# Optimization experiments

Measured on AMD Instinct MI355X. Metric: run time of the kernel, lower is better.

## Reference

```python
import jax, jax.numpy as jnp
import numpy as np
import math

B, NB, NA, NC, D, E, H = 4, 2048, 1024, 1024, 1024, 8, 16
HD = D // H
TOP_K = 2
T_MAX = 1000.0
TAU_MIN, TAU_MAX = 0.5, 2.0
W_MIN, W_MAX = 0.1, 0.2
CAP_LO, CAP_HI = 0.5, 0.6
FLOOR = min(0.05, 0.15 / E)       # cfg.routing_floor property
ALPHA = min(FLOOR * E, 1.0)       # routing-floor interpolation weight
BIAS_COEFF = 0.01
EPS = 1e-8


def _layernorm(x, g, b, eps=1e-5):
    mu = x.mean(-1, keepdims=True)
    var = ((x - mu) ** 2).mean(-1, keepdims=True)
    return (x - mu) * jax.lax.rsqrt(var + eps) * g + b


def _forward(tokens_B, output_A, output_C, in_proj_w, in_proj_b, out_proj_w, out_proj_b,
             ln_g, ln_b, te_w1, te_b1, te_w2, te_b2,
             gate_w1, gate_b1, gate_w2, gate_b2, expert_bias, t):
    t_norm = t.astype(jnp.float32) / T_MAX                 # (B,)
    ctx_C = jax.lax.stop_gradient(output_C)                # stopgrad_C_to_B
    ctx_AC = jnp.concatenate([output_A, ctx_C], axis=1)    # (B, NA+NC, D)

    # --- cross attention (torch nn.MultiheadAttention, batch_first) ---
    wq, wk, wv = jnp.split(in_proj_w, 3, axis=0)
    bq, bk, bv = jnp.split(in_proj_b, 3)
    q = (tokens_B @ wq.T + bq).reshape(B, NB, H, HD)
    k = (ctx_AC @ wk.T + bk).reshape(B, NA + NC, H, HD)
    v = (ctx_AC @ wv.T + bv).reshape(B, NA + NC, H, HD)
    scores = jnp.einsum('bqhd,bkhd->bhqk', q, k) / math.sqrt(HD)
    attn = jax.nn.softmax(scores, axis=-1)
    ctx = jnp.einsum('bhqk,bkhd->bqhd', attn, v).reshape(B, NB, D)
    ctx_B = ctx @ out_proj_w.T + out_proj_b
    ctx_B = _layernorm(ctx_B + tokens_B, ln_g, ln_b)

    # --- sinusoidal timestep embedding + 2-layer MLP ---
    half = D // 2
    freq = jnp.exp(-math.log(10000.0) * jnp.arange(half, dtype=jnp.float32) / (half - 1))
    args = t.astype(jnp.float32)[:, None] * freq
    emb = jnp.concatenate([jnp.sin(args), jnp.cos(args)], axis=-1)   # (B, D)
    t_emb = jax.nn.silu(emb @ te_w1.T + te_b1) @ te_w2.T + te_b2     # (B, D)
    t_emb = jnp.broadcast_to(t_emb[:, None, :], (B, NB, D))

    # --- gate MLP + expert bias + temperature ---
    gate_in = jnp.concatenate([tokens_B, ctx_B, t_emb], axis=-1)     # (B, NB, 3D)
    logits = jax.nn.relu(gate_in @ gate_w1.T + gate_b1) @ gate_w2.T + gate_b2 + expert_bias
    tau = (TAU_MIN + (TAU_MAX - TAU_MIN) * t_norm)[:, None, None]
    probs = jax.nn.softmax(logits / tau, axis=-1)                    # (B, NB, E)

    # routing floor: interpolate toward uniform
    probs = (1.0 - ALPHA) * probs + ALPHA / E

    # shared expert injection: expert 0 gets scheduled weight w(t), rest renormalised
    w = (W_MIN + (W_MAX - W_MIN) * t_norm)[:, None, None]
    shared = jnp.maximum(probs[..., 0:1], w)
    others = probs[..., 1:]
    others = others / jnp.maximum(others.sum(-1, keepdims=True), EPS) * (1.0 - shared)
    probs = jnp.concatenate([shared, others], axis=-1)

    # top-k mask (keep top-k probs, zero the rest)
    vals, idx = jax.lax.top_k(probs, TOP_K)
    dispatch = (jax.nn.one_hot(idx, E, dtype=probs.dtype) * vals[..., None]).sum(-2)

    # token-level hard cap (torch.no_grad -> stop_gradient) with redistribution
    cap = (CAP_LO + (CAP_HI - CAP_LO) * t_norm)[:, None, None]
    excess = jax.nn.relu(dispatch - cap)
    capped = dispatch - excess
    headroom = jax.nn.relu(cap - capped)
    head_sum = jnp.maximum(headroom.sum(-1, keepdims=True), EPS)
    capped = capped + excess.sum(-1, keepdims=True) * (headroom / head_sum)
    dispatch = jax.lax.stop_gradient(capped)

    # batch-level utilisation penalty on specialists 1..E-1
    fair = NB / max(E - 1, 1)
    load = dispatch.sum(axis=1).mean(axis=0)                          # (E,)
    pen_excess = jax.nn.relu(load[1:] - fair * 1.5)
    bias_penalty = BIAS_COEFF * jnp.sum(pen_excess ** 2)

    combine = dispatch / (dispatch.sum(-1, keepdims=True) + EPS)
    return dispatch, combine, bias_penalty


def setup_inputs() -> dict:
    key = jax.random.key(0)
    ks = jax.random.split(key, 12)
    g = lambda k, sh: jax.random.normal(k, sh, jnp.float32) * 0.02
    return dict(
        tokens_B=jax.random.normal(ks[0], (B, NB, D), jnp.float32),
        output_A=jax.random.normal(ks[1], (B, NA, D), jnp.float32),
        output_C=jax.random.normal(ks[2], (B, NC, D), jnp.float32),
        t=jax.random.randint(ks[3], (B,), 0, 1000, jnp.int32),
        in_proj_w=g(ks[4], (3 * D, D)),
        in_proj_b=jnp.zeros((3 * D,), jnp.float32),
        out_proj_w=g(ks[5], (D, D)),
        out_proj_b=jnp.zeros((D,), jnp.float32),
        ln_g=jnp.ones((D,), jnp.float32),
        ln_b=jnp.zeros((D,), jnp.float32),
        te_w1=g(ks[6], (2 * D, D)),
        te_b1=jnp.zeros((2 * D,), jnp.float32),
        te_w2=g(ks[7], (D, 2 * D)),
        te_b2=jnp.zeros((D,), jnp.float32),
        gate_w1=g(ks[8], (D, 3 * D)),
        gate_b1=jnp.zeros((D,), jnp.float32),
        gate_w2=g(ks[9], (E, D)),
        gate_b2=jnp.zeros((E,), jnp.float32),
        expert_bias=jnp.zeros((E,), jnp.float32),
    )


def reference(tokens_B, output_A, output_C, t, in_proj_w, in_proj_b, out_proj_w, out_proj_b,
              ln_g, ln_b, te_w1, te_b1, te_w2, te_b2,
              gate_w1, gate_b1, gate_w2, gate_b2, expert_bias):
    return _forward(tokens_B, output_A, output_C, in_proj_w, in_proj_b, out_proj_w, out_proj_b,
                    ln_g, ln_b, te_w1, te_b1, te_w2, te_b2,
                    gate_w1, gate_b1, gate_w2, gate_b2, expert_bias, t)
```

## Files before the change

### kernel.cpp

```cpp
#include <hip/hip_runtime.h>
#include <math.h>


typedef __attribute__((ext_vector_type(8))) short short8;
typedef __attribute__((ext_vector_type(4))) float f32x4;
typedef __attribute__((ext_vector_type(4))) unsigned int u32x4;
typedef unsigned short u16;
typedef unsigned int u32;

__global__ void zero_k(double* p) {
    if (threadIdx.x < 8) p[threadIdx.x] = 0.0;
}

__device__ inline u16 bf_hi(float x) {
    u32 u = __float_as_uint(x);
    u += 0x7FFFu + ((u >> 16) & 1u);
    return (u16)(u >> 16);
}
__device__ inline u16 bf_lo(float x, u16 h) {
    float hf = __uint_as_float(((u32)h) << 16);
    return bf_hi(x - hf);
}
__device__ inline u32 pack_bf(float x) {
    u32 u = __float_as_uint(x);
    u32 hi = (u + (0x7FFFu + ((u >> 16) & 1u))) >> 16;
    float hf = __uint_as_float(hi << 16);
    float d = x - hf;
    u32 u2 = __float_as_uint(d);
    u32 lo = (u2 + (0x7FFFu + ((u2 >> 16) & 1u))) >> 16;
    return (hi << 16) | lo;
}

__device__ inline void pack2(float p0, float p1, u32& o0, u32& o1) {
    u32 h01, l01;
    asm("v_cvt_pk_bf16_f32 %0, %1, %2" : "=v"(h01) : "v"(p0), "v"(p1));
    float d0 = p0 - __uint_as_float(h01 << 16);
    float d1 = p1 - __uint_as_float(h01 & 0xffff0000u);
    asm("v_cvt_pk_bf16_f32 %0, %1, %2" : "=v"(l01) : "v"(d0), "v"(d1));
    o0 = __builtin_amdgcn_perm(h01, l01, 0x05040100u);
    o1 = __builtin_amdgcn_perm(h01, l01, 0x07060302u);
}

__device__ inline void async16(const u16* g, u16* l) {
    __builtin_amdgcn_global_load_lds(
        (const __attribute__((address_space(1))) unsigned int*)g,
        (__attribute__((address_space(3))) unsigned int*)l,
        16, 0, 0);
}

__global__ __launch_bounds__(256)
void split_k(const float* __restrict__ in, u16* __restrict__ hi,
             u16* __restrict__ lo, int n4) {
    int i = blockIdx.x * 256 + threadIdx.x;
    if (i >= n4) return;
    float4 x = ((const float4*)in)[i];
    ushort4 h, l;
    h.x = bf_hi(x.x); l.x = bf_lo(x.x, h.x);
    h.y = bf_hi(x.y); l.y = bf_lo(x.y, h.y);
    h.z = bf_hi(x.z); l.z = bf_lo(x.z, h.z);
    h.w = bf_hi(x.w); l.w = bf_lo(x.w, h.w);
    ((ushort4*)hi)[i] = h;
    ((ushort4*)lo)[i] = l;
}

__global__ void emb_k(const int* __restrict__ t, float* __restrict__ emb) {
    int b = blockIdx.x;
    int j = threadIdx.x;
    float x1 = (float)(-9.210340371976184) * (float)j;
    float x2 = x1 / 511.0f;
    float freq = (float)exp((double)x2);
    float tf = (float)t[b];
    float arg = tf * freq;
    emb[b * 1024 + j]       = (float)sin((double)arg);
    emb[b * 1024 + 512 + j] = (float)cos((double)arg);
}

__global__ void te_fc_k(const float* __restrict__ in, const float* __restrict__ W,
                        const float* __restrict__ bias, float* __restrict__ out,
                        int K, int N, int do_silu) {
    int b = blockIdx.x;
    int wv = threadIdx.x >> 6, lane = threadIdx.x & 63;
    const float* inb = in + (size_t)b * K;
    int n0 = blockIdx.y * 16 + wv * 4;
    for (int q = 0; q < 4; q++) {
        int n = n0 + q;
        const float* wr = W + (size_t)n * K;
        float acc = 0.f;
        for (int c = lane * 4; c < K; c += 256) {
            float4 a  = *(const float4*)(inb + c);
            float4 w4 = *(const float4*)(wr + c);
            acc += a.x * w4.x + a.y * w4.y + a.z * w4.z + a.w * w4.w;
        }
#pragma unroll
        for (int off = 1; off < 64; off <<= 1) acc += __shfl_xor(acc, off, 64);
        if (lane == 0) {
            float x = acc + bias[n];
            out[(size_t)b * N + n] = do_silu ? (x / (1.0f + expf(-x))) : x;
        }
    }
}

template<bool GATE, bool RELU, int OMODE>
__global__ __launch_bounds__(256, 2)
void bfgemm_k(const u16* __restrict__ A0h, const u16* __restrict__ A0l,
              const u16* __restrict__ A1h, const u16* __restrict__ A1l,
              const u16* __restrict__ A2h, const u16* __restrict__ A2l,
              const u16* __restrict__ Wh_g, const u16* __restrict__ Wl_g,
              const float* __restrict__ bias, float* __restrict__ C,
              u16* __restrict__ Chi, u16* __restrict__ Clo, int K, float scale)
{
    __shared__ u16 Ah[128 * 32];
    __shared__ u16 Al[128 * 32];
    __shared__ u16 Wh[128 * 32];
    __shared__ u16 Wl[128 * 32];
    const int tid = threadIdx.x;
    const int row0 = blockIdx.x * 128;
    const int col0 = blockIdx.y * 128;
    const int wv = tid >> 6;
    const int lane = tid & 63;
    const int wrow = (wv & 1) * 64;
    const int wcol = (wv >> 1) * 64;
    const int l15 = lane & 15, quad = lane >> 4;

    f32x4 acc[4][4];
#pragma unroll
    for (int i = 0; i < 4; i++)
#pragma unroll
        for (int j = 0; j < 4; j++)
            acc[i][j] = (f32x4){0.f, 0.f, 0.f, 0.f};

    const int ar0 = tid >> 2, ak0 = (tid & 3) * 8;
    const int ar1 = (tid + 256) >> 2, ak1 = ((tid + 256) & 3) * 8;

    for (int kc = 0; kc < K; kc += 32) {
        const u16* pAh = A0h;
        const u16* pAl = A0l;
        int kk = kc;
        int tembseg = 0;
        if (GATE) {
            int seg = kc >> 10;
            if (seg == 1) { pAh = A1h; pAl = A1l; }
            else if (seg == 2) { pAh = A2h; pAl = A2l; tembseg = 1; }
            kk = kc & 1023;
        }
        const int astr = GATE ? 1024 : K;
        int g0 = row0 + ar0, g1 = row0 + ar1;
        if (GATE && tembseg) { g0 >>= 11; g1 >>= 11; }
        uint4 vah0 = *(const uint4*)&pAh[(size_t)g0 * astr + kk + ak0];
        uint4 vah1 = *(const uint4*)&pAh[(size_t)g1 * astr + kk + ak1];
        uint4 val0 = *(const uint4*)&pAl[(size_t)g0 * astr + kk + ak0];
        uint4 val1 = *(const uint4*)&pAl[(size_t)g1 * astr + kk + ak1];
        uint4 vwh0 = *(const uint4*)&Wh_g[(size_t)(col0 + ar0) * K + kc + ak0];
        uint4 vwh1 = *(const uint4*)&Wh_g[(size_t)(col0 + ar1) * K + kc + ak1];
        uint4 vwl0 = *(const uint4*)&Wl_g[(size_t)(col0 + ar0) * K + kc + ak0];
        uint4 vwl1 = *(const uint4*)&Wl_g[(size_t)(col0 + ar1) * K + kc + ak1];
        __syncthreads();
        *(uint4*)&Ah[ar0 * 32 + ak0] = vah0;
        *(uint4*)&Ah[ar1 * 32 + ak1] = vah1;
        *(uint4*)&Al[ar0 * 32 + ak0] = val0;
        *(uint4*)&Al[ar1 * 32 + ak1] = val1;
        *(uint4*)&Wh[ar0 * 32 + ak0] = vwh0;
        *(uint4*)&Wh[ar1 * 32 + ak1] = vwh1;
        *(uint4*)&Wl[ar0 * 32 + ak0] = vwl0;
        *(uint4*)&Wl[ar1 * 32 + ak1] = vwl1;
        __syncthreads();

        short8 a_h[4], a_l[4];
#pragma unroll
        for (int i = 0; i < 4; i++) {
            int r = (wrow + i * 16 + l15) * 32 + quad * 8;
            a_h[i] = *(const short8*)&Ah[r];
            a_l[i] = *(const short8*)&Al[r];
        }
#pragma unroll
        for (int j = 0; j < 4; j++) {
            int c = (wcol + j * 16 + l15) * 32 + quad * 8;
            short8 b_h = *(const short8*)&Wh[c];
            short8 b_l = *(const short8*)&Wl[c];
#pragma unroll
            for (int i = 0; i < 4; i++) {
                acc[i][j] = __builtin_amdgcn_mfma_f32_16x16x32_bf16(a_h[i], b_h, acc[i][j], 0, 0, 0);
                acc[i][j] = __builtin_amdgcn_mfma_f32_16x16x32_bf16(a_h[i], b_l, acc[i][j], 0, 0, 0);
                acc[i][j] = __builtin_amdgcn_mfma_f32_16x16x32_bf16(a_l[i], b_h, acc[i][j], 0, 0, 0);
            }
        }
    }

#pragma unroll
    for (int i = 0; i < 4; i++) {
#pragma unroll
        for (int j = 0; j < 4; j++) {
            int cc = col0 + wcol + j * 16 + l15;
#pragma unroll
            for (int r = 0; r < 4; r++) {
                int rr = row0 + wrow + i * 16 + quad * 4 + r;
                float v = (acc[i][j][r] + ((OMODE == 3) ? bias[rr] : bias[cc])) * scale;
                if (RELU) v = fmaxf(v, 0.f);
                if (OMODE == 0) {
                    C[(size_t)rr * 1024 + cc] = v;
                } else if (OMODE == 1) {
                    u32 pk = pack_bf(v);
                    size_t a = (size_t)rr * 1024 + cc;
                    Chi[a] = (u16)(pk >> 16); Clo[a] = (u16)pk;
                } else if (OMODE == 2) {
                    int orow = ((rr >> 10) & 3) * 2048 + (rr >> 12) * 1024 + (rr & 1023);
                    u32 pk = pack_bf(v);
                    size_t a = (size_t)orow * 1024 + cc;
                    Chi[a] = (u16)(pk >> 16); Clo[a] = (u16)pk;
                } else {
                    int bb2 = (cc >> 10) & 3;
                    int key = (cc >> 12) * 1024 + (cc & 1023);
                    u32 pk = pack_bf(v);
                    size_t a = ((size_t)(bb2 * 1024 + rr)) * 2048 + key;
                    Chi[a] = (u16)(pk >> 16); Clo[a] = (u16)pk;
                }
            }
        }
    }
}

__global__ __launch_bounds__(256)
void attn_k(const u16* Qh, const u16* Ql,
            const u16* __restrict__ Kh, const u16* __restrict__ Kl,
            const u16* __restrict__ Vh, const u16* __restrict__ Vl,
            u16* Oh, u16* Ol)
{
    __shared__ u32 Pu[128 * 64];
    __shared__ u16 Vsm[2][64 * 64];
    u16* Ksh = (u16*)Pu;
    u16* Ksl = Ksh + 64 * 64;

    const int tid = threadIdx.x;
    const int w = tid >> 6, lane = tid & 63;
    const int l15 = lane & 15, quad = lane >> 4;
    const int bh = blockIdx.x, b = bh >> 4, h = bh & 15;
    const int qw = blockIdx.y * 128 + w * 32;
    const int qrow0 = b * 2048 + qw;

    short8 qh_f[2][2], ql_f[2][2];
#pragma unroll
    for (int i = 0; i < 2; i++)
#pragma unroll
        for (int kc = 0; kc < 2; kc++) {
            size_t a = (size_t)(qrow0 + i * 16 + l15) * 1024 + h * 64 + kc * 32 + quad * 8;
            qh_f[i][kc] = *(const short8*)&Qh[a];
            ql_f[i][kc] = *(const short8*)&Ql[a];
        }

    const int srow = tid >> 3;
    const int scsw = ((tid & 7) ^ (srow & 7)) << 3;
    const size_t gk_base = ((size_t)(b * 2048) + srow) * 1024 + h * 64 + scsw;
    const size_t gv_base = ((size_t)((b * 16 + h) * 64 + srow)) * 2048 + scsw;
    u16* ldsK = Ksh + w * 512;
    u16* ldsV = &Vsm[0][0] + w * 512;

    f32x4 o[2][4];
#pragma unroll
    for (int i = 0; i < 2; i++)
#pragma unroll
        for (int j = 0; j < 4; j++) o[i][j] = (f32x4){0.f, 0.f, 0.f, 0.f};
    float lsum[2][4] = {};

    for (int kt = 0; kt < 32; kt++) {
        __syncthreads();
        {
            const size_t gk = gk_base + (size_t)kt * 65536;
            const size_t gv = gv_base + (size_t)kt * 64;
            async16(&Kh[gk],         ldsK);
            async16(&Kh[gk + 32768], ldsK + 2048);
            async16(&Kl[gk],         ldsK + 4096);
            async16(&Kl[gk + 32768], ldsK + 6144);
            async16(&Vh[gv],         ldsV);
            async16(&Vh[gv + 65536], ldsV + 2048);
            async16(&Vl[gv],         ldsV + 4096);
            async16(&Vl[gv + 65536], ldsV + 6144);
        }
        __syncthreads();
        f32x4 s[2][4];
#pragma unroll
        for (int i = 0; i < 2; i++)
#pragma unroll
            for (int j = 0; j < 4; j++) s[i][j] = (f32x4){0.f, 0.f, 0.f, 0.f};
#pragma unroll
        for (int j = 0; j < 4; j++) {
            int ka = (j * 16 + l15) * 64 + ((quad ^ (l15 & 7)) << 3);
            short8 kh0 = *(const short8*)&Ksh[ka];
            short8 kh1 = *(const short8*)&Ksh[ka ^ 32];
            short8 kl0 = *(const short8*)&Ksl[ka];
            short8 kl1 = *(const short8*)&Ksl[ka ^ 32];
#pragma unroll
            for (int i = 0; i < 2; i++) {
                s[i][j] = __builtin_amdgcn_mfma_f32_16x16x32_bf16(qh_f[i][0], kh0, s[i][j], 0, 0, 0);
                s[i][j] = __builtin_amdgcn_mfma_f32_16x16x32_bf16(qh_f[i][0], kl0, s[i][j], 0, 0, 0);
                s[i][j] = __builtin_amdgcn_mfma_f32_16x16x32_bf16(ql_f[i][0], kh0, s[i][j], 0, 0, 0);
                s[i][j] = __builtin_amdgcn_mfma_f32_16x16x32_bf16(qh_f[i][1], kh1, s[i][j], 0, 0, 0);
                s[i][j] = __builtin_amdgcn_mfma_f32_16x16x32_bf16(qh_f[i][1], kl1, s[i][j], 0, 0, 0);
                s[i][j] = __builtin_amdgcn_mfma_f32_16x16x32_bf16(ql_f[i][1], kh1, s[i][j], 0, 0, 0);
            }
        }
        __syncthreads();
#pragma unroll
        for (int i = 0; i < 2; i++)
#pragma unroll
            for (int j = 0; j < 4; j++) {
                float p0 = exp2f(s[i][j][0]);
                float p1 = exp2f(s[i][j][1]);
                float p2 = exp2f(s[i][j][2]);
                float p3 = exp2f(s[i][j][3]);
                lsum[i][0] += p0; lsum[i][1] += p1;
                lsum[i][2] += p2; lsum[i][3] += p3;
                u32 o0, o1, o2, o3;
                pack2(p0, p1, o0, o1);
                pack2(p2, p3, o2, o3);
                int rb = w * 32 + i * 16 + quad * 4;
                int csw = (j * 16 + l15) ^ ((i * 4 + quad) << 3);
                Pu[(rb + 0) * 64 + csw] = o0;
                Pu[(rb + 1) * 64 + csw] = o1;
                Pu[(rb + 2) * 64 + csw] = o2;
                Pu[(rb + 3) * 64 + csw] = o3;
            }
#pragma unroll
        for (int kc = 0; kc < 2; kc++) {
            short8 ph[2], pl[2];
#pragma unroll
            for (int i = 0; i < 2; i++) {
                int prow = w * 32 + i * 16 + l15;
                int pcol = (kc * 32 + quad * 8) ^ ((i * 4 + (l15 >> 2)) << 3);
                const uint4* pp = (const uint4*)&Pu[prow * 64 + pcol];
                uint4 u0 = pp[0], u1 = pp[1];
                union { short8 s; u32x4 u; } hh, ll;
                hh.u = (u32x4){ __builtin_amdgcn_perm(u0.y, u0.x, 0x07060302u),
                                __builtin_amdgcn_perm(u0.w, u0.z, 0x07060302u),
                                __builtin_amdgcn_perm(u1.y, u1.x, 0x07060302u),
                                __builtin_amdgcn_perm(u1.w, u1.z, 0x07060302u) };
                ll.u = (u32x4){ __builtin_amdgcn_perm(u0.y, u0.x, 0x05040100u),
                                __builtin_amdgcn_perm(u0.w, u0.z, 0x05040100u),
                                __builtin_amdgcn_perm(u1.y, u1.x, 0x05040100u),
                                __builtin_amdgcn_perm(u1.w, u1.z, 0x05040100u) };
                ph[i] = hh.s; pl[i] = ll.s;
            }
#pragma unroll
            for (int jd = 0; jd < 4; jd++) {
                int va = (jd * 16 + l15) * 64 + ((((kc << 2) + quad) ^ (l15 & 7)) << 3);
                short8 vvh = *(const short8*)&Vsm[0][va];
                short8 vvl = *(const short8*)&Vsm[1][va];
#pragma unroll
                for (int i = 0; i < 2; i++) {
                    o[i][jd] = __builtin_amdgcn_mfma_f32_16x16x32_bf16(ph[i], vvh, o[i][jd], 0, 0, 0);
                    o[i][jd] = __builtin_amdgcn_mfma_f32_16x16x32_bf16(ph[i], vvl, o[i][jd], 0, 0, 0);
                    o[i][jd] = __builtin_amdgcn_mfma_f32_16x16x32_bf16(pl[i], vvh, o[i][jd], 0, 0, 0);
                }
            }
        }
    }
#pragma unroll
    for (int i = 0; i < 2; i++)
#pragma unroll
        for (int r = 0; r < 4; r++) {
            float s2 = lsum[i][r];
            s2 += __shfl_xor(s2, 1, 64);
            s2 += __shfl_xor(s2, 2, 64);
            s2 += __shfl_xor(s2, 4, 64);
            s2 += __shfl_xor(s2, 8, 64);
            lsum[i][r] = s2;
        }
#pragma unroll
    for (int i = 0; i < 2; i++)
#pragma unroll
        for (int jd = 0; jd < 4; jd++)
#pragma unroll
            for (int r = 0; r < 4; r++) {
                float v = o[i][jd][r] / lsum[i][r];
                u32 pk = pack_bf(v);
                size_t a = (size_t)(qrow0 + i * 16 + quad * 4 + r) * 1024 + h * 64 + jd * 16 + l15;
                Oh[a] = (u16)(pk >> 16);
                Ol[a] = (u16)pk;
            }
}

__global__ __launch_bounds__(256)
void ln_split_k(const float* __restrict__ X, const float* __restrict__ T,
                const float* __restrict__ g, const float* __restrict__ bta,
                u16* __restrict__ chi, u16* __restrict__ clo)
{
    __shared__ float red[8];
    int r = blockIdx.x, tid = threadIdx.x;
    size_t base = (size_t)r * 1024 + tid * 4;
    float4 x  = *(const float4*)(X + base);
    float4 tk = *(const float4*)(T + base);
    x.x += tk.x; x.y += tk.y; x.z += tk.z; x.w += tk.w;
    float s = x.x + x.y + x.z + x.w;
#pragma unroll
    for (int off = 1; off < 64; off <<= 1) s += __shfl_xor(s, off, 64);
    int wv = tid >> 6;
    if ((tid & 63) == 0) red[wv] = s;
    __syncthreads();
    float mu = (red[0] + red[1] + red[2] + red[3]) * (1.0f / 1024.0f);
    float dx0 = x.x - mu, dx1 = x.y - mu, dx2 = x.z - mu, dx3 = x.w - mu;
    float ss = dx0 * dx0 + dx1 * dx1 + dx2 * dx2 + dx3 * dx3;
#pragma unroll
    for (int off = 1; off < 64; off <<= 1) ss += __shfl_xor(ss, off, 64);
    if ((tid & 63) == 0) red[4 + wv] = ss;
    __syncthreads();
    float var = (red[4] + red[5] + red[6] + red[7]) * (1.0f / 1024.0f);
    float inv = 1.0f / sqrtf(var + 1e-5f);
    float4 gg = *(const float4*)(g + tid * 4);
    float4 bb = *(const float4*)(bta + tid * 4);
    float y0 = dx0 * inv * gg.x + bb.x;
    float y1 = dx1 * inv * gg.y + bb.y;
    float y2 = dx2 * inv * gg.z + bb.z;
    float y3 = dx3 * inv * gg.w + bb.w;
    ushort4 h, l;
    h.x = bf_hi(y0); l.x = bf_lo(y0, h.x);
    h.y = bf_hi(y1); l.y = bf_lo(y1, h.y);
    h.z = bf_hi(y2); l.z = bf_lo(y2, h.z);
    h.w = bf_hi(y3); l.w = bf_lo(y3, h.w);
    *(ushort4*)&chi[base] = h;
    *(ushort4*)&clo[base] = l;
}

__global__ __launch_bounds__(256)
void logits_k(const float* __restrict__ Hd, const float* __restrict__ W2,
              const float* __restrict__ b2, const float* __restrict__ eb,
              float* __restrict__ Lg)
{
    int gw = (blockIdx.x * 256 + threadIdx.x) >> 6;
    int lane = threadIdx.x & 63;
    const float* h = Hd + (size_t)gw * 1024;
    float4 hv[4];
#pragma unroll
    for (int j = 0; j < 4; j++) hv[j] = *(const float4*)(h + j * 256 + lane * 4);
    float res[8];
#pragma unroll
    for (int e = 0; e < 8; e++) {
        const float* w = W2 + (size_t)e * 1024;
        float acc = 0.f;
#pragma unroll
        for (int j = 0; j < 4; j++) {
            float4 w4 = *(const float4*)(w + j * 256 + lane * 4);
            acc += hv[j].x * w4.x + hv[j].y * w4.y + hv[j].z * w4.z + hv[j].w * w4.w;
        }
#pragma unroll
        for (int off = 1; off < 64; off <<= 1) acc += __shfl_xor(acc, off, 64);
        res[e] = acc;
    }
    if (lane < 8) {
        float v = res[0];
#pragma unroll
        for (int e = 1; e < 8; e++) v = (lane == e) ? res[e] : v;
        Lg[(size_t)gw * 8 + lane] = v + b2[lane] + eb[lane];
    }
}

__global__ __launch_bounds__(256)
void router_k(const float* __restrict__ Lg, const int* __restrict__ t,
              float* __restrict__ outp, double* __restrict__ loadAcc)
{
    __shared__ double wred[4][8];
    int tid = threadIdx.x;
    int r = blockIdx.x * 256 + tid;
    int b = r >> 11;
    float tn  = (float)t[b] / 1000.0f;
    float tau = 0.5f + 1.5f * tn;
    float p[8];
    float mx = -INFINITY;
#pragma unroll
    for (int e = 0; e < 8; e++) { p[e] = Lg[(size_t)r * 8 + e] / tau; mx = fmaxf(mx, p[e]); }
    float sum = 0.f;
#pragma unroll
    for (int e = 0; e < 8; e++) { p[e] = expf(p[e] - mx); sum += p[e]; }
#pragma unroll
    for (int e = 0; e < 8; e++) p[e] = p[e] / sum;
#pragma unroll
    for (int e = 0; e < 8; e++) p[e] = 0.85f * p[e] + 0.01875f;
    float w = 0.1f + 0.1f * tn;
    float shared_p = fmaxf(p[0], w);
    float osum = 0.f;
#pragma unroll
    for (int e = 1; e < 8; e++) osum += p[e];
    float denom_o = fmaxf(osum, 1e-8f);
    float one_m = 1.0f - shared_p;
    p[0] = shared_p;
#pragma unroll
    for (int e = 1; e < 8; e++) p[e] = (p[e] / denom_o) * one_m;
    int i0 = 0; float v0 = p[0];
#pragma unroll
    for (int e = 1; e < 8; e++) if (p[e] > v0) { v0 = p[e]; i0 = e; }
    int i1 = -1; float v1 = -INFINITY;
#pragma unroll
    for (int e = 0; e < 8; e++) if (e != i0 && p[e] > v1) { v1 = p[e]; i1 = e; }
    float cap = 0.5f + 0.1f * tn;
    float dsp[8], capped[8], hr[8];
    float exsum = 0.f, hsum = 0.f;
#pragma unroll
    for (int e = 0; e < 8; e++) {
        float d = ((e == i0) ? v0 : 0.f) + ((e == i1) ? v1 : 0.f);
        float ex = fmaxf(d - cap, 0.f);
        float c = d - ex;
        float hh = fmaxf(cap - c, 0.f);
        capped[e] = c; hr[e] = hh;
        exsum += ex; hsum += hh;
    }
    float hden = fmaxf(hsum, 1e-8f);
    float dsum = 0.f;
#pragma unroll
    for (int e = 0; e < 8; e++) {
        float d = capped[e] + exsum * (hr[e] / hden);
        dsp[e] = d; dsum += d;
    }
    float cden = dsum + 1e-8f;
#pragma unroll
    for (int e = 0; e < 8; e++) {
        outp[(size_t)r * 8 + e] = dsp[e];
        outp[65536 + (size_t)r * 8 + e] = dsp[e] / cden;
    }
    int lane = tid & 63, wv = tid >> 6;
#pragma unroll
    for (int e = 0; e < 8; e++) {
        double s = (double)dsp[e];
#pragma unroll
        for (int off = 1; off < 64; off <<= 1) s += __shfl_xor(s, off, 64);
        if (lane == 0) wred[wv][e] = s;
    }
    __syncthreads();
    if (tid < 8) {
        double s = wred[0][tid] + wred[1][tid] + wred[2][tid] + wred[3][tid];
        atomicAdd(&loadAcc[tid], s);
    }
}

__global__ void penalty_k(const double* __restrict__ loadAcc, float* __restrict__ outp) {
    if (threadIdx.x == 0) {
        const float thr = (float)(2048.0 / 7.0 * 1.5);
        float pen = 0.f;
#pragma unroll
        for (int e = 1; e < 8; e++) {
            float load = (float)(loadAcc[e] / 4.0);
            float x = fmaxf(load - thr, 0.f);
            pen += x * x;
        }
        outp[131072] = 0.01f * pen;
    }
}

extern "C" void kernel_launch(void* const* d_in, const int* in_sizes, int n_in,
                              void* d_out, int out_size, void* d_ws, size_t ws_size,
                              hipStream_t stream)
{
    const float* tokens = (const float*)d_in[0];
    const float* outA   = (const float*)d_in[1];
    const float* outC   = (const float*)d_in[2];
    const int*   tt     = (const int*)  d_in[3];
    const float* in_w   = (const float*)d_in[4];
    const float* in_b   = (const float*)d_in[5];
    const float* op_w   = (const float*)d_in[6];
    const float* op_b   = (const float*)d_in[7];
    const float* lng    = (const float*)d_in[8];
    const float* lnb    = (const float*)d_in[9];
    const float* te_w1  = (const float*)d_in[10];
    const float* te_b1  = (const float*)d_in[11];
    const float* te_w2  = (const float*)d_in[12];
    const float* te_b2  = (const float*)d_in[13];
    const float* g_w1   = (const float*)d_in[14];
    const float* g_b1   = (const float*)d_in[15];
    const float* g_w2   = (const float*)d_in[16];
    const float* g_b2   = (const float*)d_in[17];
    const float* e_bias = (const float*)d_in[18];
    float* out = (float*)d_out;

    float* ws = (float*)d_ws;
    const size_t NM = (size_t)8192 * 1024;
    float* F0     = ws;
    float* temb   = ws + NM;
    float* embb   = temb + 4096;
    float* hte    = embb + 4096;
    float* logitsb = hte + 8192;
    double* loads = (double*)(logitsb + 65536);

    u16* U = (u16*)(loads + 16);
    u16* Tokh = U;
    u16* Tokl = Tokh + NM;
    u16* ActH = Tokl + NM;
    u16* ActL = ActH + NM;
    u16* Qh   = ActL + NM;
    u16* Ql   = Qh + NM;
    u16* Kh   = Ql + NM;
    u16* Kl   = Kh + NM;
    u16* Vth  = Kl + NM;
    u16* Vtl  = Vth + NM;
    u16* Wsh  = Vtl + NM;
    u16* Wsl  = Wsh + (size_t)3 * 1024 * 1024;
    u16* Tbh  = Wsl + (size_t)3 * 1024 * 1024;
    u16* Tbl  = Tbh + 4096;

    zero_k<<<1, 64, 0, stream>>>(loads);
    emb_k<<<4, 512, 0, stream>>>(tt, embb);
    te_fc_k<<<dim3(4, 128), 256, 0, stream>>>(embb, te_w1, te_b1, hte, 1024, 2048, 1);
    te_fc_k<<<dim3(4, 64),  256, 0, stream>>>(hte,  te_w2, te_b2, temb, 2048, 1024, 0);

    split_k<<<8192, 256, 0, stream>>>(tokens, Tokh, Tokl, 8192 * 1024 / 4);
    split_k<<<3072, 256, 0, stream>>>(in_w, Wsh, Wsl, 3 * 1024 * 1024 / 4);
    split_k<<<4096, 256, 0, stream>>>(outA, ActH, ActL, 4096 * 1024 / 4);
    split_k<<<4096, 256, 0, stream>>>(outC, ActH + (size_t)4096 * 1024,
                                      ActL + (size_t)4096 * 1024, 4096 * 1024 / 4);

    bfgemm_k<false, false, 1><<<dim3(64, 8), 256, 0, stream>>>(
        Tokh, Tokl, nullptr, nullptr, nullptr, nullptr,
        Wsh, Wsl, in_b, nullptr, Qh, Ql, 1024, 0.18033688011112042f);
    bfgemm_k<false, false, 2><<<dim3(64, 8), 256, 0, stream>>>(
        ActH, ActL, nullptr, nullptr, nullptr, nullptr,
        Wsh + (size_t)1024 * 1024, Wsl + (size_t)1024 * 1024,
        in_b + 1024, nullptr, Kh, Kl, 1024, 1.0f);
    bfgemm_k<false, false, 3><<<dim3(8, 64), 256, 0, stream>>>(
        Wsh + (size_t)2048 * 1024, Wsl + (size_t)2048 * 1024,
        nullptr, nullptr, nullptr, nullptr,
        ActH, ActL, in_b + 2048, nullptr, Vth, Vtl, 1024, 1.0f);

    attn_k<<<dim3(64, 16), 256, 0, stream>>>(Qh, Ql, Kh, Kl, Vth, Vtl, Qh, Ql);

    split_k<<<1024, 256, 0, stream>>>(op_w, Wsh, Wsl, 1024 * 1024 / 4);
    bfgemm_k<false, false, 0><<<dim3(64, 8), 256, 0, stream>>>(
        Qh, Ql, nullptr, nullptr, nullptr, nullptr,
        Wsh, Wsl, op_b, F0, nullptr, nullptr, 1024, 1.0f);

    ln_split_k<<<8192, 256, 0, stream>>>(F0, tokens, lng, lnb, Kh, Kl);

    split_k<<<4, 256, 0, stream>>>(temb, Tbh, Tbl, 4096 / 4);
    split_k<<<3072, 256, 0, stream>>>(g_w1, Wsh, Wsl, 3072 * 1024 / 4);
    bfgemm_k<true, true, 0><<<dim3(64, 8), 256, 0, stream>>>(
        Tokh, Tokl, Kh, Kl, Tbh, Tbl,
        Wsh, Wsl, g_b1, F0, nullptr, nullptr, 3072, 1.0f);

    logits_k<<<2048, 256, 0, stream>>>(F0, g_w2, g_b2, e_bias, logitsb);
    router_k<<<32, 256, 0, stream>>>(logitsb, tt, out, loads);
    penalty_k<<<1, 64, 0, stream>>>(loads, out);
}
```

Baseline: 859.0 us.

## Double-buffer K/V tiles and enlarge attention blocks to 512 threads

The attention kernel now uses 8 waves per block covering 256 query rows. Each K/V tile is loaded once per block and prefetched into a second LDS buffer while the current tile is computed, which removes two of the three barriers per iteration. The P-tile LDS swizzle is also changed to reduce bank conflicts. LDS use grows to about 128KB, which limits occupancy to one block per CU and halves the grid.

```diff
diff --git a/kernel.cpp b/kernel.cpp
--- a/kernel.cpp
+++ b/kernel.cpp
@@ -219,22 +219,21 @@
     }
 }
 
-__global__ __launch_bounds__(256)
+__global__ __launch_bounds__(512)
 void attn_k(const u16* Qh, const u16* Ql,
             const u16* __restrict__ Kh, const u16* __restrict__ Kl,
             const u16* __restrict__ Vh, const u16* __restrict__ Vl,
             u16* Oh, u16* Ol)
 {
-    __shared__ u32 Pu[128 * 64];
-    __shared__ u16 Vsm[2][64 * 64];
-    u16* Ksh = (u16*)Pu;
-    u16* Ksl = Ksh + 64 * 64;
+    __shared__ u32 Pu[256 * 64];
+    __shared__ u16 Kb[2][2][64 * 64];
+    __shared__ u16 Vb[2][2][64 * 64];
 
     const int tid = threadIdx.x;
     const int w = tid >> 6, lane = tid & 63;
     const int l15 = lane & 15, quad = lane >> 4;
     const int bh = blockIdx.x, b = bh >> 4, h = bh & 15;
-    const int qw = blockIdx.y * 128 + w * 32;
+    const int qw = blockIdx.y * 256 + w * 32;
     const int qrow0 = b * 2048 + qw;
 
     short8 qh_f[2][2], ql_f[2][2];
@@ -251,31 +250,43 @@
     const int scsw = ((tid & 7) ^ (srow & 7)) << 3;
     const size_t gk_base = ((size_t)(b * 2048) + srow) * 1024 + h * 64 + scsw;
     const size_t gv_base = ((size_t)((b * 16 + h) * 64 + srow)) * 2048 + scsw;
-    u16* ldsK = Ksh + w * 512;
-    u16* ldsV = &Vsm[0][0] + w * 512;
 
     f32x4 o[2][4];
 #pragma unroll
     for (int i = 0; i < 2; i++)
 #pragma unroll
         for (int j = 0; j < 4; j++) o[i][j] = (f32x4){0.f, 0.f, 0.f, 0.f};
-    float lsum[2][4] = {};
+    float lsum[2] = {0.f, 0.f};
+    float lsv[2][4] = {};
+
+    {
+        u16* kd = &Kb[0][0][0] + w * 512;
+        u16* vd = &Vb[0][0][0] + w * 512;
+        async16(&Kh[gk_base], kd);
+        async16(&Kl[gk_base], kd + 4096);
+        async16(&Vh[gv_base], vd);
+        async16(&Vl[gv_base], vd + 4096);
+    }
+    __syncthreads();
 
     for (int kt = 0; kt < 32; kt++) {
-        __syncthreads();
-        {
-            const size_t gk = gk_base + (size_t)kt * 65536;
-            const size_t gv = gv_base + (size_t)kt * 64;
-            async16(&Kh[gk],         ldsK);
-            async16(&Kh[gk + 32768], ldsK + 2048);
-            async16(&Kl[gk],         ldsK + 4096);
-            async16(&Kl[gk + 32768], ldsK + 6144);
-            async16(&Vh[gv],         ldsV);
-            async16(&Vh[gv + 65536], ldsV + 2048);
-            async16(&Vl[gv],         ldsV + 4096);
-            async16(&Vl[gv + 65536], ldsV + 6144);
-        }
-        __syncthreads();
+        const int cur = kt & 1;
+        if (kt < 31) {
+            const int nxt = cur ^ 1;
+            const size_t gk = gk_base + (size_t)(kt + 1) * 65536;
+            const size_t gv = gv_base + (size_t)(kt + 1) * 64;
+            u16* kd = &Kb[0][0][0] + nxt * 8192 + w * 512;
+            u16* vd = &Vb[0][0][0] + nxt * 8192 + w * 512;
+            async16(&Kh[gk], kd);
+            async16(&Kl[gk], kd + 4096);
+            async16(&Vh[gv], vd);
+            async16(&Vl[gv], vd + 4096);
+        }
+        const u16* Ksh = &Kb[0][0][0] + cur * 8192;
+        const u16* Ksl = Ksh + 4096;
+        const u16* Vs0 = &Vb[0][0][0] + cur * 8192;
+        const u16* Vs1 = Vs0 + 4096;
+
         f32x4 s[2][4];
 #pragma unroll
         for (int i = 0; i < 2; i++)
@@ -298,7 +309,6 @@
                 s[i][j] = __builtin_amdgcn_mfma_f32_16x16x32_bf16(ql_f[i][1], kh1, s[i][j], 0, 0, 0);
             }
         }
-        __syncthreads();
 #pragma unroll
         for (int i = 0; i < 2; i++)
 #pragma unroll
@@ -307,17 +317,18 @@
                 float p1 = exp2f(s[i][j][1]);
                 float p2 = exp2f(s[i][j][2]);
                 float p3 = exp2f(s[i][j][3]);
-                lsum[i][0] += p0; lsum[i][1] += p1;
-                lsum[i][2] += p2; lsum[i][3] += p3;
+                lsv[i][0] += p0; lsv[i][1] += p1;
+                lsv[i][2] += p2; lsv[i][3] += p3;
                 u32 o0, o1, o2, o3;
                 pack2(p0, p1, o0, o1);
                 pack2(p2, p3, o2, o3);
                 int rb = w * 32 + i * 16 + quad * 4;
-                int csw = (j * 16 + l15) ^ ((i * 4 + quad) << 3);
-                Pu[(rb + 0) * 64 + csw] = o0;
-                Pu[(rb + 1) * 64 + csw] = o1;
-                Pu[(rb + 2) * 64 + csw] = o2;
-                Pu[(rb + 3) * 64 + csw] = o3;
+                int cq = (j * 4 + (l15 >> 2)) ^ ((quad & 1) << 2);
+                int off = l15 & 3;
+                Pu[(rb + 0) * 64 + ((cq ^ 0) << 2) + off] = o0;
+                Pu[(rb + 1) * 64 + ((cq ^ 1) << 2) + off] = o1;
+                Pu[(rb + 2) * 64 + ((cq ^ 2) << 2) + off] = o2;
+                Pu[(rb + 3) * 64 + ((cq ^ 3) << 2) + off] = o3;
             }
 #pragma unroll
         for (int kc = 0; kc < 2; kc++) {
@@ -325,9 +336,11 @@
 #pragma unroll
             for (int i = 0; i < 2; i++) {
                 int prow = w * 32 + i * 16 + l15;
-                int pcol = (kc * 32 + quad * 8) ^ ((i * 4 + (l15 >> 2)) << 3);
-                const uint4* pp = (const uint4*)&Pu[prow * 64 + pcol];
-                uint4 u0 = pp[0], u1 = pp[1];
+                int x = l15 & 7;
+                int k0 = kc * 8 + quad * 2;
+                const u32* basep = &Pu[prow * 64];
+                uint4 u0 = *(const uint4*)&basep[(k0 ^ x) << 2];
+                uint4 u1 = *(const uint4*)&basep[((k0 + 1) ^ x) << 2];
                 union { short8 s; u32x4 u; } hh, ll;
                 hh.u = (u32x4){ __builtin_amdgcn_perm(u0.y, u0.x, 0x07060302u),
                                 __builtin_amdgcn_perm(u0.w, u0.z, 0x07060302u),
@@ -342,8 +355,8 @@
 #pragma unroll
             for (int jd = 0; jd < 4; jd++) {
                 int va = (jd * 16 + l15) * 64 + ((((kc << 2) + quad) ^ (l15 & 7)) << 3);
-                short8 vvh = *(const short8*)&Vsm[0][va];
-                short8 vvl = *(const short8*)&Vsm[1][va];
+                short8 vvh = *(const short8*)&Vs0[va];
+                short8 vvl = *(const short8*)&Vs1[va];
 #pragma unroll
                 for (int i = 0; i < 2; i++) {
                     o[i][jd] = __builtin_amdgcn_mfma_f32_16x16x32_bf16(ph[i], vvh, o[i][jd], 0, 0, 0);
@@ -352,25 +365,27 @@
                 }
             }
         }
+        __syncthreads();
     }
 #pragma unroll
     for (int i = 0; i < 2; i++)
 #pragma unroll
         for (int r = 0; r < 4; r++) {
-            float s2 = lsum[i][r];
+            float s2 = lsv[i][r];
             s2 += __shfl_xor(s2, 1, 64);
             s2 += __shfl_xor(s2, 2, 64);
             s2 += __shfl_xor(s2, 4, 64);
             s2 += __shfl_xor(s2, 8, 64);
-            lsum[i][r] = s2;
-        }
+            lsv[i][r] = s2;
+        }
+    (void)lsum;
 #pragma unroll
     for (int i = 0; i < 2; i++)
 #pragma unroll
         for (int jd = 0; jd < 4; jd++)
 #pragma unroll
             for (int r = 0; r < 4; r++) {
-                float v = o[i][jd][r] / lsum[i][r];
+                float v = o[i][jd][r] / lsv[i][r];
                 u32 pk = pack_bf(v);
                 size_t a = (size_t)(qrow0 + i * 16 + quad * 4 + r) * 1024 + h * 64 + jd * 16 + l15;
                 Oh[a] = (u16)(pk >> 16);
@@ -616,7 +631,7 @@
         nullptr, nullptr, nullptr, nullptr,
         ActH, ActL, in_b + 2048, nullptr, Vth, Vtl, 1024, 1.0f);
 
-    attn_k<<<dim3(64, 16), 256, 0, stream>>>(Qh, Ql, Kh, Kl, Vth, Vtl, Qh, Ql);
+    attn_k<<<dim3(64, 8), 512, 0, stream>>>(Qh, Ql, Kh, Kl, Vth, Vtl, Qh, Ql);
 
     split_k<<<1024, 256, 0, stream>>>(op_w, Wsh, Wsl, 1024 * 1024 / 4);
     bfgemm_k<false, false, 0><<<dim3(64, 8), 256, 0, stream>>>(
```

After: 825.6 us. 1.04x faster.
